# Optimization experiments

Hardware: AMD Instinct MI355X
Metric: run time of the kernel (lower is better)

Reference implementation:

```python
import jax, jax.numpy as jnp
import numpy as np

EPS = 0.001  # iso_score epsilon from the module


def setup_inputs() -> dict:
    key = jax.random.key(0)
    ks = jax.random.split(key, 8)
    B, N, T = 8, 50000, 64
    E = 1_600_000
    hidden, horizon = 256, 24
    x = jax.random.normal(ks[0], (B, N, T, 1), dtype=jnp.float32)
    edge_index = jax.random.randint(ks[1], (2, E), 0, N, dtype=jnp.int32)
    edge_weight = jax.random.uniform(ks[2], (E,), dtype=jnp.float32)
    gcn_weight = jax.random.normal(ks[3], (hidden,), dtype=jnp.float32) * (1.0)  # GCNConv lin weight, in_dim=1
    gcn_bias = jax.random.normal(ks[4], (hidden,), dtype=jnp.float32) * 0.02
    proj_weight = jax.random.normal(ks[5], (hidden, horizon), dtype=jnp.float32) * (hidden ** -0.5)
    proj_bias = jax.random.normal(ks[6], (horizon,), dtype=jnp.float32) * 0.02
    return {"x": x, "edge_index": edge_index, "edge_weight": edge_weight,
            "gcn_weight": gcn_weight, "gcn_bias": gcn_bias,
            "proj_weight": proj_weight, "proj_bias": proj_bias}


def reference(x, edge_index, edge_weight, gcn_weight, gcn_bias, proj_weight, proj_bias):
    B, N, T, _ = x.shape
    src, dst = edge_index[0], edge_index[1]

    # iso_score = 1 / (weighted out-degree + eps), from __init__ (bincount over edge_index[0])
    deg_w = jax.ops.segment_sum(edge_weight, src, num_segments=N)  # [N]
    iso = 1.0 / (deg_w + EPS)

    x_mean = x.mean(axis=2)[..., 0]        # [B, N]
    xw = x_mean * iso                       # [B, N]

    # PyG GCNConv with add_self_loops=True, edge weights = 1 (none passed in forward)
    loop = jnp.arange(N, dtype=src.dtype)
    row = jnp.concatenate([src, loop])      # sources j
    col = jnp.concatenate([dst, loop])      # targets i
    deg = jax.ops.segment_sum(jnp.ones(row.shape[0], x.dtype), col, num_segments=N)
    dinv = jnp.where(deg > 0, jax.lax.rsqrt(deg), 0.0)
    norm = dinv[row] * dinv[col]            # [E+N]

    # GCN is linear: aggregate scalar features first, then expand with weight
    msg = xw[:, row] * norm[None, :]        # [B, E+N]
    agg = jax.vmap(lambda m: jax.ops.segment_sum(m, col, num_segments=N))(msg)  # [B, N]
    h = agg[..., None] * gcn_weight + gcn_bias   # [B, N, hidden]

    return h @ proj_weight + proj_bias           # [B, N, horizon]
```

## Files before the change

### kernel.cpp

```cpp
#include <hip/hip_runtime.h>

constexpr int B = 8;
constexpr int N = 50000;
constexpr int T = 64;
constexpr int E = 1600000;
constexpr int HIDDEN = 256;
constexpr int HOR = 24;
constexpr int CAP = 96;
#define EPS 0.001f

__global__ void fill_kernel(const int* __restrict__ ei, const float* __restrict__ ew,
                            float* __restrict__ deg_w, int* __restrict__ cursor,
                            int* __restrict__ csr) {
    int e = blockIdx.x * blockDim.x + threadIdx.x;
    if (e >= E) return;
    int s = ei[e];
    int d = ei[E + e];
    unsafeAtomicAdd(&deg_w[s], ew[e]);
    int pos = atomicAdd(&cursor[d], 1);
    if (pos < CAP) csr[d * CAP + pos] = s;
}

__global__ void prep_kernel(const float* __restrict__ deg_w, const int* __restrict__ cursor,
                            float* __restrict__ iso, float* __restrict__ dinv) {
    int n = blockIdx.x * blockDim.x + threadIdx.x;
    if (n >= N) return;
    iso[n]  = 1.0f / (deg_w[n] + EPS);
    dinv[n] = rsqrtf((float)(cursor[n] + 1));
}

__global__ void xmean_kernel(const float* __restrict__ x, const float* __restrict__ iso,
                             float* __restrict__ xwt) {
    int tid = blockIdx.x * blockDim.x + threadIdx.x;
    int p = tid >> 4;
    int l = tid & 15;
    if (p >= B * N) return;
    float4 v = ((const float4*)x)[(size_t)p * 16 + l];
    float sum = v.x + v.y + v.z + v.w;
    sum += __shfl_xor(sum, 1);
    sum += __shfl_xor(sum, 2);
    sum += __shfl_xor(sum, 4);
    sum += __shfl_xor(sum, 8);
    if (l == 0) {
        int n = p % N;
        int b = p / N;
        xwt[(size_t)n * B + b] = (sum * (1.0f / 64.0f)) * iso[n];
    }
}

__global__ void wc_kernel(const float* __restrict__ gw, const float* __restrict__ gb,
                          const float* __restrict__ pw, const float* __restrict__ pb,
                          float* __restrict__ wc) {
    int k = threadIdx.x;
    if (k >= HOR) return;
    float w = 0.0f, c = 0.0f;
    for (int h = 0; h < HIDDEN; ++h) {
        float p = pw[h * HOR + k];
        w += gw[h] * p;
        c += gb[h] * p;
    }
    wc[k] = w;
    wc[HOR + k] = c + pb[k];
}

__global__ void gather_kernel(const int* __restrict__ cursor, const int* __restrict__ csr,
                              const float* __restrict__ dinv, const float* __restrict__ xwt,
                              float* __restrict__ sacc) {
    int tid = blockIdx.x * blockDim.x + threadIdx.x;
    int d = tid >> 6;
    int lane = tid & 63;
    if (d >= N) return;
    int cnt = cursor[d];
    if (cnt > CAP) cnt = CAP;
    int b  = lane & 7;
    int jo = lane >> 3;
    const int* list = csr + d * CAP;
    float acc = 0.0f;
    for (int j = jo; j < cnt; j += 8) {
        int s = list[j];
        acc += xwt[(size_t)s * 8 + b] * dinv[s];
    }
    acc += __shfl_xor(acc, 8);
    acc += __shfl_xor(acc, 16);
    acc += __shfl_xor(acc, 32);
    if (lane < 8) {
        float dvd = dinv[d];
        sacc[(size_t)d * 8 + b] = acc * dvd + xwt[(size_t)d * 8 + b] * dvd * dvd;
    }
}

__global__ void out_kernel(const float* __restrict__ sacc, const float* __restrict__ wc,
                           float* __restrict__ out) {
    int idx = blockIdx.x * blockDim.x + threadIdx.x;
    if (idx >= B * N * HOR) return;
    int p = idx / HOR;
    int k = idx - p * HOR;
    int n = p % N;
    int b = p / N;
    float agg = sacc[(size_t)n * 8 + b];
    out[idx] = agg * wc[k] + wc[HOR + k];
}

extern "C" void kernel_launch(void* const* d_in, const int* in_sizes, int n_in,
                              void* d_out, int out_size, void* d_ws, size_t ws_size,
                              hipStream_t stream) {
    const float* x  = (const float*)d_in[0];
    const int*   ei = (const int*)d_in[1];
    const float* ew = (const float*)d_in[2];
    const float* gw = (const float*)d_in[3];
    const float* gb = (const float*)d_in[4];
    const float* pw = (const float*)d_in[5];
    const float* pb = (const float*)d_in[6];
    float* out = (float*)d_out;

    char* ws = (char*)d_ws;
    float* deg_w  = (float*)ws;
    int*   cursor = (int*)(ws + (size_t)N * 4);
    float* iso    = (float*)(ws + (size_t)2 * N * 4);
    float* dinv   = (float*)(ws + (size_t)3 * N * 4);
    float* xwt    = (float*)(ws + (size_t)4 * N * 4);
    float* sacc   = (float*)(ws + (size_t)12 * N * 4);
    float* wc     = (float*)(ws + (size_t)20 * N * 4);
    int*   csr    = (int*)(ws + (size_t)20 * N * 4 + 256);

    hipMemsetAsync(ws, 0, (size_t)2 * N * 4, stream);

    fill_kernel<<<(E + 255) / 256, 256, 0, stream>>>(ei, ew, deg_w, cursor, csr);
    prep_kernel<<<(N + 255) / 256, 256, 0, stream>>>(deg_w, cursor, iso, dinv);
    xmean_kernel<<<(B * N * 16 + 255) / 256, 256, 0, stream>>>(x, iso, xwt);
    wc_kernel<<<1, 32, 0, stream>>>(gw, gb, pw, pb, wc);
    gather_kernel<<<(N * 64 + 255) / 256, 256, 0, stream>>>(cursor, csr, dinv, xwt, sacc);
    out_kernel<<<(B * N * HOR + 255) / 256, 256, 0, stream>>>(sacc, wc, out);
}
```

Measured before the change: 399.4 us.

## Fuse six kernels into three, folding iso scaling and output projection into gather

Merges the edge fill and x-mean passes into one launch with block-range dispatch, so the x-mean no longer waits for iso. Moves the iso scaling into per-node factors f and g computed in prep, and folds the weight-combine kernel into prep's last block. Fuses the output projection into the gather kernel so each node writes its 8x24 outputs directly, which removes the sacc round trip and the separate out launch. The cost is that output stores are now 24-float strided chunks per batch rather than fully linear, and the exact-division grid sizes assume the dimensions divide evenly.

Result: faster. 370.8 us (-7.2%).

```diff
diff --git a/kernel.cpp b/kernel.cpp
--- a/kernel.cpp
+++ b/kernel.cpp
@@ -7,69 +7,73 @@
 constexpr int HIDDEN = 256;
 constexpr int HOR = 24;
 constexpr int CAP = 96;
+constexpr int FILL_BLOCKS = E / 256;
+constexpr int XMEAN_BLOCKS = B * N * 16 / 256;
 #define EPS 0.001f
 
-__global__ void fill_kernel(const int* __restrict__ ei, const float* __restrict__ ew,
-                            float* __restrict__ deg_w, int* __restrict__ cursor,
-                            int* __restrict__ csr) {
-    int e = blockIdx.x * blockDim.x + threadIdx.x;
-    if (e >= E) return;
-    int s = ei[e];
-    int d = ei[E + e];
-    unsafeAtomicAdd(&deg_w[s], ew[e]);
-    int pos = atomicAdd(&cursor[d], 1);
-    if (pos < CAP) csr[d * CAP + pos] = s;
+__global__ void fill_xmean_kernel(const int* __restrict__ ei, const float* __restrict__ ew,
+                                  const float* __restrict__ x,
+                                  float* __restrict__ deg_w, int* __restrict__ cursor,
+                                  int* __restrict__ csr, float* __restrict__ xm) {
+    int bid = blockIdx.x;
+    if (bid < FILL_BLOCKS) {
+        int e = bid * 256 + threadIdx.x;
+        int s = ei[e];
+        int d = ei[E + e];
+        unsafeAtomicAdd(&deg_w[s], ew[e]);
+        int pos = atomicAdd(&cursor[d], 1);
+        if (pos < CAP) csr[d * CAP + pos] = s;
+    } else {
+        int tid = (bid - FILL_BLOCKS) * 256 + threadIdx.x;
+        int p = tid >> 4;
+        int l = tid & 15;
+        float4 v = ((const float4*)x)[(size_t)p * 16 + l];
+        float sum = v.x + v.y + v.z + v.w;
+        sum += __shfl_xor(sum, 1);
+        sum += __shfl_xor(sum, 2);
+        sum += __shfl_xor(sum, 4);
+        sum += __shfl_xor(sum, 8);
+        if (l == 0) {
+            int n = p % N;
+            int b = p / N;
+            xm[(size_t)n * B + b] = sum * (1.0f / 64.0f);
+        }
+    }
 }
 
 __global__ void prep_kernel(const float* __restrict__ deg_w, const int* __restrict__ cursor,
-                            float* __restrict__ iso, float* __restrict__ dinv) {
-    int n = blockIdx.x * blockDim.x + threadIdx.x;
-    if (n >= N) return;
-    iso[n]  = 1.0f / (deg_w[n] + EPS);
-    dinv[n] = rsqrtf((float)(cursor[n] + 1));
-}
-
-__global__ void xmean_kernel(const float* __restrict__ x, const float* __restrict__ iso,
-                             float* __restrict__ xwt) {
-    int tid = blockIdx.x * blockDim.x + threadIdx.x;
-    int p = tid >> 4;
-    int l = tid & 15;
-    if (p >= B * N) return;
-    float4 v = ((const float4*)x)[(size_t)p * 16 + l];
-    float sum = v.x + v.y + v.z + v.w;
-    sum += __shfl_xor(sum, 1);
-    sum += __shfl_xor(sum, 2);
-    sum += __shfl_xor(sum, 4);
-    sum += __shfl_xor(sum, 8);
-    if (l == 0) {
-        int n = p % N;
-        int b = p / N;
-        xwt[(size_t)n * B + b] = (sum * (1.0f / 64.0f)) * iso[n];
+                            const float* __restrict__ gw, const float* __restrict__ gb,
+                            const float* __restrict__ pw, const float* __restrict__ pb,
+                            float* __restrict__ dinv, float* __restrict__ f,
+                            float* __restrict__ g, float* __restrict__ wcv) {
+    int n = blockIdx.x * 256 + threadIdx.x;
+    if (n < N) {
+        float iso = 1.0f / (deg_w[n] + EPS);
+        float dv = rsqrtf((float)(cursor[n] + 1));
+        dinv[n] = dv;
+        f[n] = iso * dv;
+        g[n] = iso * dv * dv;
+    }
+    if (blockIdx.x == gridDim.x - 1 && threadIdx.x >= 128 && threadIdx.x < 128 + HOR) {
+        int k = threadIdx.x - 128;
+        float w = 0.0f, c = 0.0f;
+        for (int h = 0; h < HIDDEN; ++h) {
+            float p = pw[h * HOR + k];
+            w += gw[h] * p;
+            c += gb[h] * p;
+        }
+        wcv[k] = w;
+        wcv[HOR + k] = c + pb[k];
     }
 }
 
-__global__ void wc_kernel(const float* __restrict__ gw, const float* __restrict__ gb,
-                          const float* __restrict__ pw, const float* __restrict__ pb,
-                          float* __restrict__ wc) {
-    int k = threadIdx.x;
-    if (k >= HOR) return;
-    float w = 0.0f, c = 0.0f;
-    for (int h = 0; h < HIDDEN; ++h) {
-        float p = pw[h * HOR + k];
-        w += gw[h] * p;
-        c += gb[h] * p;
-    }
-    wc[k] = w;
-    wc[HOR + k] = c + pb[k];
-}
-
-__global__ void gather_kernel(const int* __restrict__ cursor, const int* __restrict__ csr,
-                              const float* __restrict__ dinv, const float* __restrict__ xwt,
-                              float* __restrict__ sacc) {
-    int tid = blockIdx.x * blockDim.x + threadIdx.x;
+__global__ void gather_out_kernel(const int* __restrict__ cursor, const int* __restrict__ csr,
+                                  const float* __restrict__ dinv, const float* __restrict__ f,
+                                  const float* __restrict__ g, const float* __restrict__ xm,
+                                  const float* __restrict__ wcv, float* __restrict__ out) {
+    int tid = blockIdx.x * 256 + threadIdx.x;
     int d = tid >> 6;
     int lane = tid & 63;
-    if (d >= N) return;
     int cnt = cursor[d];
     if (cnt > CAP) cnt = CAP;
     int b  = lane & 7;
@@ -78,27 +82,23 @@
     float acc = 0.0f;
     for (int j = jo; j < cnt; j += 8) {
         int s = list[j];
-        acc += xwt[(size_t)s * 8 + b] * dinv[s];
+        acc += xm[(size_t)s * 8 + b] * f[s];
     }
     acc += __shfl_xor(acc, 8);
     acc += __shfl_xor(acc, 16);
     acc += __shfl_xor(acc, 32);
-    if (lane < 8) {
-        float dvd = dinv[d];
-        sacc[(size_t)d * 8 + b] = acc * dvd + xwt[(size_t)d * 8 + b] * dvd * dvd;
-    }
-}
-
-__global__ void out_kernel(const float* __restrict__ sacc, const float* __restrict__ wc,
-                           float* __restrict__ out) {
-    int idx = blockIdx.x * blockDim.x + threadIdx.x;
-    if (idx >= B * N * HOR) return;
-    int p = idx / HOR;
-    int k = idx - p * HOR;
-    int n = p % N;
-    int b = p / N;
-    float agg = sacc[(size_t)n * 8 + b];
-    out[idx] = agg * wc[k] + wc[HOR + k];
+    int bg = lane >> 3;
+    float aggb = __shfl(acc, bg);
+    float dvd = dinv[d];
+    aggb = aggb * dvd + xm[(size_t)d * 8 + bg] * g[d];
+    int k0 = lane & 7;
+    float o0 = aggb * wcv[k0]      + wcv[HOR + k0];
+    float o1 = aggb * wcv[k0 + 8]  + wcv[HOR + k0 + 8];
+    float o2 = aggb * wcv[k0 + 16] + wcv[HOR + k0 + 16];
+    size_t base = (size_t)bg * N * HOR + (size_t)d * HOR;
+    out[base + k0]      = o0;
+    out[base + k0 + 8]  = o1;
+    out[base + k0 + 16] = o2;
 }
 
 extern "C" void kernel_launch(void* const* d_in, const int* in_sizes, int n_in,
@@ -116,19 +116,19 @@
     char* ws = (char*)d_ws;
     float* deg_w  = (float*)ws;
     int*   cursor = (int*)(ws + (size_t)N * 4);
-    float* iso    = (float*)(ws + (size_t)2 * N * 4);
-    float* dinv   = (float*)(ws + (size_t)3 * N * 4);
-    float* xwt    = (float*)(ws + (size_t)4 * N * 4);
-    float* sacc   = (float*)(ws + (size_t)12 * N * 4);
-    float* wc     = (float*)(ws + (size_t)20 * N * 4);
-    int*   csr    = (int*)(ws + (size_t)20 * N * 4 + 256);
+    float* dinv   = (float*)(ws + (size_t)2 * N * 4);
+    float* f      = (float*)(ws + (size_t)3 * N * 4);
+    float* g      = (float*)(ws + (size_t)4 * N * 4);
+    float* xm     = (float*)(ws + (size_t)5 * N * 4);
+    float* wcv    = (float*)(ws + (size_t)13 * N * 4);
+    int*   csr    = (int*)(ws + (size_t)13 * N * 4 + 256);
 
     hipMemsetAsync(ws, 0, (size_t)2 * N * 4, stream);
 
-    fill_kernel<<<(E + 255) / 256, 256, 0, stream>>>(ei, ew, deg_w, cursor, csr);
-    prep_kernel<<<(N + 255) / 256, 256, 0, stream>>>(deg_w, cursor, iso, dinv);
-    xmean_kernel<<<(B * N * 16 + 255) / 256, 256, 0, stream>>>(x, iso, xwt);
-    wc_kernel<<<1, 32, 0, stream>>>(gw, gb, pw, pb, wc);
-    gather_kernel<<<(N * 64 + 255) / 256, 256, 0, stream>>>(cursor, csr, dinv, xwt, sacc);
-    out_kernel<<<(B * N * HOR + 255) / 256, 256, 0, stream>>>(sacc, wc, out);
+    fill_xmean_kernel<<<FILL_BLOCKS + XMEAN_BLOCKS, 256, 0, stream>>>(
+        ei, ew, x, deg_w, cursor, csr, xm);
+    prep_kernel<<<(N + 255) / 256, 256, 0, stream>>>(
+        deg_w, cursor, gw, gb, pw, pb, dinv, f, g, wcv);
+    gather_out_kernel<<<N * 64 / 256, 256, 0, stream>>>(
+        cursor, csr, dinv, f, g, xm, wcv, out);
 }
```
